# Optimization experiments

Measured on AMD Instinct MI355X. Metric: run time of the kernel, lower is better.

The kernel has to match this reference:

```python
import jax, jax.numpy as jnp
import numpy as np

L, S, R, NUM_RESNET = 6, 2, 3, 3
N = 2 ** L            # 64 blocks per axis
NX = N * S            # 128 grid points per axis
NCART_SIDE = 80
NCART = NCART_SIDE ** 2


def _perm_idx(L_, l):
    delta = 2 ** (L_ - l - 1)
    t = np.tile(np.arange(2) * delta, delta) + np.repeat(np.arange(delta), 2)
    t = np.tile(t, 2 ** l) + np.repeat(np.arange(2 ** l) * 2 ** (L_ - l), 2 ** (L_ - l))
    return jnp.asarray(t)


def _switch_idx(L_):
    h = L_ // 2
    t = np.tile(np.arange(2 ** h) * 2 ** h, 2 ** h) + np.repeat(np.arange(2 ** h), 2 ** h)
    return jnp.asarray(t)


def _bmm2(x, g_left, g_right):
    # x: (B,p,i,q,j). Right block-diag GEMM on (q,j), then left block-diag GEMM on (p,i).
    y = jnp.einsum('bpiqj,qjk->bpiqk', x, g_right)
    return jnp.einsum('bpiqk,pio->bpoqk', y, g_left)


def _complex_layer(xr, xi, p):
    # p: stacked (r1,i1,r2,i2,r3,i3,r4,i4); complex-style cross products of the original.
    r1, i1, r2, i2, r3, i3, r4, i4 = p
    yr = _bmm2(xr, r1, r1) + _bmm2(xr, i1, i1) + _bmm2(xi, r2, i2) + _bmm2(xi, i2, r2)
    yi = _bmm2(xi, r3, r3) + _bmm2(xi, i3, i3) + _bmm2(xr, r4, i4) + _bmm2(xr, i4, r4)
    return yr, yi


def _u_layer(xr, xi, p):
    ur1, ui1, ur2, ui2, ur3, ui3, ur4, ui4 = p
    return (_bmm2(xr, ur1, ur1) + _bmm2(xr, ui2, ui2)
            + _bmm2(xi, ur3, ui3) + _bmm2(xi, ui4, ur4))


def _permute(yr, yi, idx):
    yr = jnp.take(jnp.take(yr, idx, axis=1), idx, axis=3)
    yi = jnp.take(jnp.take(yi, idx, axis=1), idx, axis=3)
    return yr, yi


def _merge(y):  # (B,N,R,N,R) -> (B,N/2,2R,N/2,2R)
    return y.reshape(y.shape[0], N // 2, 2 * R, N // 2, 2 * R)


def _split(y):  # inverse of _merge
    return y.reshape(y.shape[0], N, R, N, R)


def reference(x, Vp, Hp, Mp, Gp, Up, cart_mat, r_index):
    B = x.shape[0]
    xr = x[..., 0].reshape(B, N, S, N, S)
    xi = x[..., 1].reshape(B, N, S, N, S)
    yr, yi = _complex_layer(xr, xi, Vp)                       # (B,N,R,N,R)
    for li, l in enumerate(range(L - 1, L // 2 - 1, -1)):     # H stages (permute then merge-GEMM)
        yr, yi = _permute(yr, yi, _perm_idx(L, l))
        yr, yi = _complex_layer(_merge(yr), _merge(yi), Hp[li])
        yr, yi = _split(yr), _split(yi)
    yr, yi = _permute(yr, yi, _switch_idx(L))                 # middle switch shuffle
    for k in range(NUM_RESNET):                               # residual M blocks
        zr, zi = _complex_layer(yr, yi, Mp[k])
        yr, yi = yr + zr, yi + zi
    for li, l in enumerate(range(L // 2 - 1, -1, -1)):        # G stages (merge-GEMM then permute)
        yr, yi = _complex_layer(_merge(yr), _merge(yi), Gp[li])
        yr, yi = _split(yr), _split(yi)
        yr, yi = _permute(yr, yi, _perm_idx(L, l))
    y = _u_layer(yr, yi, Up).reshape(B, NX * NX)              # real output, (B,NX,NX) flattened
    y = jnp.take(y, r_index, axis=1)                          # polar reindexing
    out = y @ cart_mat.T                                      # polar -> cartesian interpolation
    return out.reshape(B, NCART_SIDE, NCART_SIDE)


def setup_inputs() -> dict:
    key = jax.random.key(0)
    ks = jax.random.split(key, 9)
    B = 128
    x = jax.random.normal(ks[0], (B, NX, NX, 2), dtype=jnp.float32)
    Vp = jax.random.normal(ks[1], (8, N, S, R), dtype=jnp.float32) * 0.35
    Hp = jax.random.normal(ks[2], (L // 2, 8, N // 2, 2 * R, 2 * R), dtype=jnp.float32) * 0.2
    Mp = jax.random.normal(ks[3], (NUM_RESNET, 8, N, R, R), dtype=jnp.float32) * 0.25
    Gp = jax.random.normal(ks[4], (L // 2, 8, N // 2, 2 * R, 2 * R), dtype=jnp.float32) * 0.2
    Up = jax.random.normal(ks[5], (8, N, R, S), dtype=jnp.float32) * 0.35
    cart_mat = jax.random.normal(ks[6], (NCART, NX * NX), dtype=jnp.float32) * 0.01
    r_index = jax.random.permutation(ks[7], NX * NX).astype(jnp.int32)
    return {"x": x, "Vp": Vp, "Hp": Hp, "Mp": Mp, "Gp": Gp, "Up": Up,
            "cart_mat": cart_mat, "r_index": r_index}
```

## Files before the change

### kernel.cpp

```cpp
#include <hip/hip_runtime.h>


typedef __attribute__((ext_vector_type(8))) short sx8;
typedef __attribute__((ext_vector_type(4))) float fx4;
typedef __attribute__((ext_vector_type(8))) unsigned short usx8;
typedef __attribute__((ext_vector_type(4))) unsigned short usx4;

__device__ __forceinline__ unsigned short f2bf(float f) {
  unsigned u = __builtin_bit_cast(unsigned, f);
  u = (u + 0x7FFFu + ((u >> 16) & 1u)) >> 16;
  return (unsigned short)u;
}
__device__ __forceinline__ float bf2f(unsigned short h) {
  return __builtin_bit_cast(float, ((unsigned)h) << 16);
}

template<int ID>
__device__ __forceinline__ int rp_apply(int k) {
  if constexpr (ID == 0) { return k; }
  else if constexpr (ID == 3) { return (k & 7) * 8 + (k >> 3); }
  else {
    constexpr int l = (ID == 1) ? 4 : (ID == 2) ? 3 : (ID == 4) ? 2 : (ID == 5) ? 1 : 0;
    constexpr int d = 1 << (5 - l);
    constexpr int m2 = 2 * d;
    int g = k / m2, r = k % m2;
    return g * m2 + (r & 1) * d + (r >> 1);
  }
}

__global__ __launch_bounds__(256) void k_transpose(const float* __restrict__ x,
                                                   float* __restrict__ xtr,
                                                   float* __restrict__ xti) {
  __shared__ float ls[2][32][129];
  const int t = threadIdx.x;
  const int u = blockIdx.x;
  const int v0 = blockIdx.y * 32;
  for (int it = 0; it < 32; ++it) {
    int b = it * 4 + (t >> 6);
    int r = t & 63;
    int v = r >> 1, ch = r & 1;
    ls[ch][v][b] = x[(((size_t)b * 128 + u) * 128 + (v0 + v)) * 2 + ch];
  }
  __syncthreads();
  for (int it = 0; it < 32; ++it) {
    int idx = it * 256 + t;
    int ch = idx >> 12;
    int v = (idx >> 7) & 31;
    int b = idx & 127;
    float* dst = ch ? xti : xtr;
    dst[((size_t)(u * 128 + v0 + v)) * 128 + b] = ls[ch][v][b];
  }
}

__global__ __launch_bounds__(128) void k_vh(const float* __restrict__ xtr,
                                            const float* __restrict__ xti,
                                            float* __restrict__ yr,
                                            float* __restrict__ yi,
                                            const float* __restrict__ vp,
                                            const float* __restrict__ hp) {
  const int b = threadIdx.x;
  const int P = blockIdx.x, Q = blockIdx.y;
  float Vr[36], Vi[36];

#pragma unroll
  for (int pp = 0; pp < 2; ++pp)
#pragma unroll
    for (int qq = 0; qq < 2; ++qq) {
      const int p = 2 * P + pp, q = 2 * Q + qq;
      float Xr[4], Xi[4];
#pragma unroll
      for (int i = 0; i < 2; ++i)
#pragma unroll
        for (int j = 0; j < 2; ++j) {
          size_t off = ((size_t)((4 * P + 2 * pp + i) * 128 + (4 * Q + 2 * qq + j))) * 128 + b;
          Xr[i * 2 + j] = xtr[off];
          Xi[i * 2 + j] = xti[off];
        }
      float Ar[9], Ai[9];
#pragma unroll
      for (int k = 0; k < 9; ++k) { Ar[k] = 0.f; Ai[k] = 0.f; }
      auto termV = [&](float* Y, const float* X, int lm, int rm) {
        const float* Lw = vp + ((size_t)lm * 64 + p) * 6;
        const float* Rw = vp + ((size_t)rm * 64 + q) * 6;
#pragma unroll
        for (int i = 0; i < 2; ++i) {
          float t0 = X[i*2+0] * Rw[0] + X[i*2+1] * Rw[3];
          float t1 = X[i*2+0] * Rw[1] + X[i*2+1] * Rw[4];
          float t2 = X[i*2+0] * Rw[2] + X[i*2+1] * Rw[5];
#pragma unroll
          for (int o = 0; o < 3; ++o) {
            float lv = Lw[i * 3 + o];
            Y[o*3+0] += lv * t0; Y[o*3+1] += lv * t1; Y[o*3+2] += lv * t2;
          }
        }
      };
      termV(Ar, Xr, 0, 0); termV(Ar, Xr, 1, 1); termV(Ai, Xr, 6, 7); termV(Ai, Xr, 7, 6);
      termV(Ar, Xi, 2, 3); termV(Ar, Xi, 3, 2); termV(Ai, Xi, 4, 4); termV(Ai, Xi, 5, 5);
#pragma unroll
      for (int o = 0; o < 3; ++o)
#pragma unroll
        for (int k = 0; k < 3; ++k) {
          Vr[(3 * pp + o) * 6 + 3 * qq + k] = Ar[o * 3 + k];
          Vi[(3 * pp + o) * 6 + 3 * qq + k] = Ai[o * 3 + k];
        }
    }

  float Yr[36], Yi[36];
#pragma unroll
  for (int k = 0; k < 36; ++k) { Yr[k] = 0.f; Yi[k] = 0.f; }
  auto termH = [&](float* Y, const float* X, int lm, int rm) {
    const float* Lw = hp + ((size_t)lm * 32 + P) * 36;
    const float* Rw = hp + ((size_t)rm * 32 + Q) * 36;
#pragma unroll
    for (int i = 0; i < 6; ++i) {
      float tk[6];
#pragma unroll
      for (int k = 0; k < 6; ++k) tk[k] = 0.f;
#pragma unroll
      for (int j = 0; j < 6; ++j) {
        float xv = X[i * 6 + j];
#pragma unroll
        for (int k = 0; k < 6; ++k) tk[k] += xv * Rw[j * 6 + k];
      }
#pragma unroll
      for (int o = 0; o < 6; ++o) {
        float lv = Lw[i * 6 + o];
#pragma unroll
        for (int k = 0; k < 6; ++k) Y[o * 6 + k] += lv * tk[k];
      }
    }
  };
  termH(Yr, Vr, 0, 0); termH(Yr, Vr, 1, 1); termH(Yi, Vr, 6, 7); termH(Yi, Vr, 7, 6);
  termH(Yr, Vi, 2, 3); termH(Yr, Vi, 3, 2); termH(Yi, Vi, 4, 4); termH(Yi, Vi, 5, 5);

#pragma unroll
  for (int I = 0; I < 6; ++I)
#pragma unroll
    for (int J = 0; J < 6; ++J) {
      size_t off = ((size_t)((P * 6 + I) * 192 + (Q * 6 + J))) * 128 + b;
      yr[off] = Yr[I * 6 + J];
      yi[off] = Yi[I * 6 + J];
    }
}

template<int PERM>
__global__ __launch_bounds__(128) void k_hg(const float* __restrict__ xr,
                                            const float* __restrict__ xi,
                                            float* __restrict__ yr,
                                            float* __restrict__ yi,
                                            const float* __restrict__ wp) {
  const int b = threadIdx.x;
  const int P = blockIdx.x, Q = blockIdx.y;
  int rrow[6], rcol[6];
#pragma unroll
  for (int I = 0; I < 6; ++I) {
    rrow[I] = rp_apply<PERM>(2 * P + I / 3) * 3 + I % 3;
    rcol[I] = rp_apply<PERM>(2 * Q + I / 3) * 3 + I % 3;
  }
  float X[36], Yr[36], Yi[36];
#pragma unroll
  for (int k = 0; k < 36; ++k) { Yr[k] = 0.f; Yi[k] = 0.f; }

  auto loadX = [&](const float* src) {
#pragma unroll
    for (int I = 0; I < 6; ++I)
#pragma unroll
      for (int J = 0; J < 6; ++J)
        X[I * 6 + J] = src[((size_t)(rrow[I] * 192 + rcol[J])) * 128 + b];
  };
  auto term = [&](float* Y, int lm, int rm) {
    const float* Lw = wp + ((size_t)lm * 32 + P) * 36;
    const float* Rw = wp + ((size_t)rm * 32 + Q) * 36;
#pragma unroll
    for (int i = 0; i < 6; ++i) {
      float tk[6];
#pragma unroll
      for (int k = 0; k < 6; ++k) tk[k] = 0.f;
#pragma unroll
      for (int j = 0; j < 6; ++j) {
        float xv = X[i * 6 + j];
#pragma unroll
        for (int k = 0; k < 6; ++k) tk[k] += xv * Rw[j * 6 + k];
      }
#pragma unroll
      for (int o = 0; o < 6; ++o) {
        float lv = Lw[i * 6 + o];
#pragma unroll
        for (int k = 0; k < 6; ++k) Y[o * 6 + k] += lv * tk[k];
      }
    }
  };
  loadX(xr);
  term(Yr, 0, 0); term(Yr, 1, 1); term(Yi, 6, 7); term(Yi, 7, 6);
  loadX(xi);
  term(Yr, 2, 3); term(Yr, 3, 2); term(Yi, 4, 4); term(Yi, 5, 5);
#pragma unroll
  for (int I = 0; I < 6; ++I)
#pragma unroll
    for (int J = 0; J < 6; ++J) {
      size_t off = ((size_t)((P * 6 + I) * 192 + (Q * 6 + J))) * 128 + b;
      yr[off] = Yr[I * 6 + J];
      yi[off] = Yi[I * 6 + J];
    }
}

__global__ __launch_bounds__(128) void k_mg(const float* __restrict__ xr,
                                            const float* __restrict__ xi,
                                            float* __restrict__ yr,
                                            float* __restrict__ yi,
                                            const float* __restrict__ mp,
                                            const float* __restrict__ gp) {
  const int b = threadIdx.x;
  const int P = blockIdx.x, Q = blockIdx.y;
  float Vr[36], Vi[36];

#pragma unroll
  for (int aa = 0; aa < 2; ++aa)
#pragma unroll
    for (int bb = 0; bb < 2; ++bb) {
      const int p = 2 * P + aa, q = 2 * Q + bb;
      const int prow = rp_apply<3>(p) * 3, pcol = rp_apply<3>(q) * 3;
      float Xr[9], Xi[9];
#pragma unroll
      for (int i = 0; i < 3; ++i)
#pragma unroll
        for (int j = 0; j < 3; ++j) {
          size_t off = ((size_t)((prow + i) * 192 + (pcol + j))) * 128 + b;
          Xr[i * 3 + j] = xr[off];
          Xi[i * 3 + j] = xi[off];
        }
#pragma unroll
      for (int lk = 0; lk < 3; ++lk) {
        const float* wp = mp + (size_t)lk * (8 * 64 * 9);
        float Yr9[9], Yi9[9];
#pragma unroll
        for (int k = 0; k < 9; ++k) { Yr9[k] = Xr[k]; Yi9[k] = Xi[k]; }
        auto termM = [&](float* Y, const float* X, int lm, int rm) {
          const float* Lw = wp + ((size_t)lm * 64 + p) * 9;
          const float* Rw = wp + ((size_t)rm * 64 + q) * 9;
#pragma unroll
          for (int i = 0; i < 3; ++i) {
            float t0 = X[i*3+0] * Rw[0] + X[i*3+1] * Rw[3] + X[i*3+2] * Rw[6];
            float t1 = X[i*3+0] * Rw[1] + X[i*3+1] * Rw[4] + X[i*3+2] * Rw[7];
            float t2 = X[i*3+0] * Rw[2] + X[i*3+1] * Rw[5] + X[i*3+2] * Rw[8];
#pragma unroll
            for (int o = 0; o < 3; ++o) {
              float lv = Lw[i * 3 + o];
              Y[o*3+0] += lv * t0; Y[o*3+1] += lv * t1; Y[o*3+2] += lv * t2;
            }
          }
        };
        termM(Yr9, Xr, 0, 0); termM(Yr9, Xr, 1, 1); termM(Yi9, Xr, 6, 7); termM(Yi9, Xr, 7, 6);
        termM(Yr9, Xi, 2, 3); termM(Yr9, Xi, 3, 2); termM(Yi9, Xi, 4, 4); termM(Yi9, Xi, 5, 5);
#pragma unroll
        for (int k = 0; k < 9; ++k) { Xr[k] = Yr9[k]; Xi[k] = Yi9[k]; }
      }
#pragma unroll
      for (int i = 0; i < 3; ++i)
#pragma unroll
        for (int j = 0; j < 3; ++j) {
          Vr[(3 * aa + i) * 6 + 3 * bb + j] = Xr[i * 3 + j];
          Vi[(3 * aa + i) * 6 + 3 * bb + j] = Xi[i * 3 + j];
        }
    }

  float Yr[36], Yi[36];
#pragma unroll
  for (int k = 0; k < 36; ++k) { Yr[k] = 0.f; Yi[k] = 0.f; }
  auto termH = [&](float* Y, const float* X, int lm, int rm) {
    const float* Lw = gp + ((size_t)lm * 32 + P) * 36;
    const float* Rw = gp + ((size_t)rm * 32 + Q) * 36;
#pragma unroll
    for (int i = 0; i < 6; ++i) {
      float tk[6];
#pragma unroll
      for (int k = 0; k < 6; ++k) tk[k] = 0.f;
#pragma unroll
      for (int j = 0; j < 6; ++j) {
        float xv = X[i * 6 + j];
#pragma unroll
        for (int k = 0; k < 6; ++k) tk[k] += xv * Rw[j * 6 + k];
      }
#pragma unroll
      for (int o = 0; o < 6; ++o) {
        float lv = Lw[i * 6 + o];
#pragma unroll
        for (int k = 0; k < 6; ++k) Y[o * 6 + k] += lv * tk[k];
      }
    }
  };
  termH(Yr, Vr, 0, 0); termH(Yr, Vr, 1, 1); termH(Yi, Vr, 6, 7); termH(Yi, Vr, 7, 6);
  termH(Yr, Vi, 2, 3); termH(Yr, Vi, 3, 2); termH(Yi, Vi, 4, 4); termH(Yi, Vi, 5, 5);

#pragma unroll
  for (int I = 0; I < 6; ++I)
#pragma unroll
    for (int J = 0; J < 6; ++J) {
      size_t off = ((size_t)((P * 6 + I) * 192 + (Q * 6 + J))) * 128 + b;
      yr[off] = Yr[I * 6 + J];
      yi[off] = Yi[I * 6 + J];
    }
}

__global__ __launch_bounds__(128) void k_u(const float* __restrict__ xr,
                                           const float* __restrict__ xi,
                                           unsigned short* __restrict__ ut,
                                           const float* __restrict__ wp) {
  const int b = threadIdx.x;
  const int p = blockIdx.x, q = blockIdx.y;
  int rrow[3], rcol[3];
#pragma unroll
  for (int i = 0; i < 3; ++i) {
    rrow[i] = rp_apply<6>(p) * 3 + i;
    rcol[i] = rp_apply<6>(q) * 3 + i;
  }
  float X[9], Y[4] = {0.f, 0.f, 0.f, 0.f};
  auto loadX = [&](const float* src) {
#pragma unroll
    for (int i = 0; i < 3; ++i)
#pragma unroll
      for (int j = 0; j < 3; ++j)
        X[i * 3 + j] = src[((size_t)(rrow[i] * 192 + rcol[j])) * 128 + b];
  };
  auto term = [&](int lm, int rm) {
    const float* Lw = wp + ((size_t)lm * 64 + p) * 6;
    const float* Rw = wp + ((size_t)rm * 64 + q) * 6;
#pragma unroll
    for (int i = 0; i < 3; ++i) {
      float t0 = X[i*3+0] * Rw[0] + X[i*3+1] * Rw[2] + X[i*3+2] * Rw[4];
      float t1 = X[i*3+0] * Rw[1] + X[i*3+1] * Rw[3] + X[i*3+2] * Rw[5];
      Y[0] += Lw[i*2+0] * t0; Y[1] += Lw[i*2+0] * t1;
      Y[2] += Lw[i*2+1] * t0; Y[3] += Lw[i*2+1] * t1;
    }
  };
  loadX(xr); term(0, 0); term(3, 3);
  loadX(xi); term(4, 5); term(7, 6);
#pragma unroll
  for (int o = 0; o < 2; ++o)
#pragma unroll
    for (int k = 0; k < 2; ++k)
      ut[((size_t)((p * 2 + o) * 128 + (q * 2 + k))) * 128 + b] = f2bf(Y[o * 2 + k]);
}

__global__ __launch_bounds__(256) void k_gather(const unsigned short* __restrict__ ut,
                                                const int* __restrict__ r_index,
                                                unsigned short* __restrict__ yg) {
  __shared__ unsigned short ls[64][130];
  __shared__ int ridx[64];
  const int t = threadIdx.x;
  const int m0 = blockIdx.x * 64;
  if (t < 64) ridx[t] = r_index[m0 + t];
  __syncthreads();
  for (int it = 0; it < 32; ++it) {
    int idx = it * 256 + t;
    int ml = idx >> 7, b = idx & 127;
    ls[ml][b] = ut[(size_t)ridx[ml] * 128 + b];
  }
  __syncthreads();
  int b = t >> 1, half = t & 1;
#pragma unroll
  for (int c = 0; c < 4; ++c) {
    usx8 v;
#pragma unroll
    for (int e = 0; e < 8; ++e) v[e] = ls[half * 32 + c * 8 + e][b];
    *(usx8*)(yg + (size_t)b * 16384 + m0 + half * 32 + c * 8) = v;
  }
}

#define GEMM_KC 16
#define GEMM_NKS 32

__global__ __launch_bounds__(256) void k_gemm(const unsigned short* __restrict__ yg,
                                              const float* __restrict__ cart,
                                              unsigned short* __restrict__ partial) {
  __shared__ unsigned short As[2][128][40];
  __shared__ unsigned short Bs[2][128][40];
  const int t = threadIdx.x;
  const int lane = t & 63, w = t >> 6;
  const int wm = w >> 1, wn = w & 1;
  const int c0 = blockIdx.x * 128;
  const int k0 = blockIdx.y * 1024;
  const int kc = blockIdx.y;

  fx4 acc[4][4];
#pragma unroll
  for (int i = 0; i < 4; ++i)
#pragma unroll
    for (int j = 0; j < 4; ++j) acc[i][j] = (fx4)0.f;

  auto ldA = [&](int rep, int kpos) -> usx8 {
    int c = t + rep * 256;
    return *(const usx8*)(yg + (size_t)(c >> 2) * 16384 + kpos + (c & 3) * 8);
  };
  auto stA = [&](int buf, int rep, usx8 v) {
    int c = t + rep * 256;
    *(usx8*)(&As[buf][c >> 2][(c & 3) * 8]) = v;
  };
  auto ldB = [&](int rep, int kpos) -> fx4 {
    int c = t + rep * 256;
    return *(const fx4*)(cart + (size_t)(c0 + (c >> 3)) * 16384 + kpos + (c & 7) * 4);
  };
  auto stB = [&](int buf, int rep, fx4 f) {
    int c = t + rep * 256;
    usx4 v;
    v[0] = f2bf(f[0]); v[1] = f2bf(f[1]); v[2] = f2bf(f[2]); v[3] = f2bf(f[3]);
    *(usx4*)(&Bs[buf][c >> 3][(c & 7) * 4]) = v;
  };

  {
    usx8 a0 = ldA(0, k0), a1 = ldA(1, k0);
    fx4 b0 = ldB(0, k0), b1 = ldB(1, k0), b2 = ldB(2, k0), b3 = ldB(3, k0);
    stA(0, 0, a0); stA(0, 1, a1);
    stB(0, 0, b0); stB(0, 1, b1); stB(0, 2, b2); stB(0, 3, b3);
  }
  __syncthreads();

  for (int s = 0; s < GEMM_NKS; ++s) {
    const int cur = s & 1;
    usx8 av0, av1; fx4 bv0, bv1, bv2, bv3;
    const bool pf = (s + 1 < GEMM_NKS);
    if (pf) {
      int kpos = k0 + (s + 1) * 32;
      av0 = ldA(0, kpos); av1 = ldA(1, kpos);
      bv0 = ldB(0, kpos); bv1 = ldB(1, kpos); bv2 = ldB(2, kpos); bv3 = ldB(3, kpos);
    }
    sx8 af[4], bfr[4];
#pragma unroll
    for (int mi = 0; mi < 4; ++mi) {
      int row = wm * 64 + mi * 16 + (lane & 15);
      af[mi] = *(const sx8*)(&As[cur][row][(lane >> 4) * 8]);
    }
#pragma unroll
    for (int ni = 0; ni < 4; ++ni) {
      int row = wn * 64 + ni * 16 + (lane & 15);
      bfr[ni] = *(const sx8*)(&Bs[cur][row][(lane >> 4) * 8]);
    }
#pragma unroll
    for (int mi = 0; mi < 4; ++mi)
#pragma unroll
      for (int ni = 0; ni < 4; ++ni)
        acc[mi][ni] = __builtin_amdgcn_mfma_f32_16x16x32_bf16(af[mi], bfr[ni], acc[mi][ni], 0, 0, 0);
    if (pf) {
      stA(cur ^ 1, 0, av0); stA(cur ^ 1, 1, av1);
      stB(cur ^ 1, 0, bv0); stB(cur ^ 1, 1, bv1); stB(cur ^ 1, 2, bv2); stB(cur ^ 1, 3, bv3);
    }
    __syncthreads();
  }

#pragma unroll
  for (int mi = 0; mi < 4; ++mi) {
    int brow = wm * 64 + mi * 16 + (lane >> 4) * 4;
#pragma unroll
    for (int ni = 0; ni < 4; ++ni) {
      int cc = c0 + wn * 64 + ni * 16 + (lane & 15);
#pragma unroll
      for (int r = 0; r < 4; ++r)
        partial[((size_t)kc * 128 + brow + r) * 6400 + cc] = f2bf(acc[mi][ni][r]);
    }
  }
}

__global__ __launch_bounds__(256) void k_reduce(const unsigned short* __restrict__ partial,
                                                float* __restrict__ out) {
  int i = blockIdx.x * 256 + threadIdx.x;
  fx4 s = (fx4)0.f;
#pragma unroll
  for (int kc = 0; kc < GEMM_KC; ++kc) {
    usx4 v = *(const usx4*)(partial + (size_t)kc * 819200 + (size_t)i * 4);
    s[0] += bf2f(v[0]); s[1] += bf2f(v[1]); s[2] += bf2f(v[2]); s[3] += bf2f(v[3]);
  }
  *(fx4*)(out + (size_t)i * 4) = s;
}

extern "C" void kernel_launch(void* const* d_in, const int* in_sizes, int n_in,
                              void* d_out, int out_size, void* d_ws, size_t ws_size,
                              hipStream_t stream) {
  const float* x    = (const float*)d_in[0];
  const float* Vp   = (const float*)d_in[1];
  const float* Hp   = (const float*)d_in[2];
  const float* Mp   = (const float*)d_in[3];
  const float* Gp   = (const float*)d_in[4];
  const float* Up   = (const float*)d_in[5];
  const float* cart = (const float*)d_in[6];
  const int*   ridx = (const int*)d_in[7];
  float* out = (float*)d_out;
  float* ws  = (float*)d_ws;

  const size_t PSZ = 4718592;
  float* P0r = ws;
  float* P0i = ws + PSZ;
  float* P1r = ws + 2 * PSZ;
  float* P1i = ws + 3 * PSZ;
  float* xtr = ws + 4 * PSZ;
  float* xti = xtr + 2097152;
  unsigned short* ut = (unsigned short*)(ws + 4 * PSZ);
  unsigned short* yg = (unsigned short*)(ws + 4 * PSZ + 1048576);
  unsigned short* partial = (unsigned short*)ws;

  const size_t HSZ = 8 * 32 * 36;

  k_transpose<<<dim3(128, 4), 256, 0, stream>>>(x, xtr, xti);
  k_vh<<<dim3(32, 32), 128, 0, stream>>>(xtr, xti, P0r, P0i, Vp, Hp + 0 * HSZ);
  k_hg<1><<<dim3(32, 32), 128, 0, stream>>>(P0r, P0i, P1r, P1i, Hp + 1 * HSZ);
  k_hg<2><<<dim3(32, 32), 128, 0, stream>>>(P1r, P1i, P0r, P0i, Hp + 2 * HSZ);
  k_mg<<<dim3(32, 32), 128, 0, stream>>>(P0r, P0i, P1r, P1i, Mp, Gp + 0 * HSZ);
  k_hg<4><<<dim3(32, 32), 128, 0, stream>>>(P1r, P1i, P0r, P0i, Gp + 1 * HSZ);
  k_hg<5><<<dim3(32, 32), 128, 0, stream>>>(P0r, P0i, P1r, P1i, Gp + 2 * HSZ);
  k_u<<<dim3(64, 64), 128, 0, stream>>>(P1r, P1i, ut, Up);
  k_gather<<<dim3(256), 256, 0, stream>>>(ut, ridx, yg);
  k_gemm<<<dim3(50, GEMM_KC), 256, 0, stream>>>(yg, cart, partial);
  k_reduce<<<dim3(800), 256, 0, stream>>>(partial, out);
  (void)in_sizes; (void)n_in; (void)out_size; (void)ws_size;
}
```

Measured before the change: 360.4 us.

## Retile final GEMM with narrower N tiles, deeper K steps, fewer fp32 split-K partials

The polar-to-cartesian GEMM is re-tiled from 128x128 output tiles with 16-way split-K to 128x64 tiles with 4-way split-K and a K step of 64 per stage. Each wave now owns a 32-row strip, and partials are stored as fp32 instead of bf16, which shrinks the reduce to four reads per element. The aim is to cut partial-sum traffic and make better use of the cart matrix loads. The trade-off is a grid of 400 blocks instead of 800, and each A tile is reused across only 64 columns, so yg is re-read more often.

```diff
diff --git a/kernel.cpp b/kernel.cpp
--- a/kernel.cpp
+++ b/kernel.cpp
@@ -367,108 +367,114 @@
   }
 }
 
-#define GEMM_KC 16
-#define GEMM_NKS 32
-
-__global__ __launch_bounds__(256) void k_gemm(const unsigned short* __restrict__ yg,
-                                              const float* __restrict__ cart,
-                                              unsigned short* __restrict__ partial) {
-  __shared__ unsigned short As[2][128][40];
-  __shared__ unsigned short Bs[2][128][40];
+#define G2_KC 4
+#define G2_STEPS 64
+#define G2_PITCH 72
+
+__global__ __launch_bounds__(256) void k_gemm2(const unsigned short* __restrict__ yg,
+                                               const float* __restrict__ cart,
+                                               float* __restrict__ partial) {
+  __shared__ unsigned short As[2][128][G2_PITCH];
+  __shared__ unsigned short Bs[2][64][G2_PITCH];
   const int t = threadIdx.x;
   const int lane = t & 63, w = t >> 6;
-  const int wm = w >> 1, wn = w & 1;
-  const int c0 = blockIdx.x * 128;
-  const int k0 = blockIdx.y * 1024;
-  const int kc = blockIdx.y;
-
-  fx4 acc[4][4];
-#pragma unroll
-  for (int i = 0; i < 4; ++i)
+  const int kc = blockIdx.x;
+  const int c0 = blockIdx.y * 64;
+  const int k0 = kc * 4096;
+
+  fx4 acc[2][4];
+#pragma unroll
+  for (int i = 0; i < 2; ++i)
 #pragma unroll
     for (int j = 0; j < 4; ++j) acc[i][j] = (fx4)0.f;
 
   auto ldA = [&](int rep, int kpos) -> usx8 {
     int c = t + rep * 256;
-    return *(const usx8*)(yg + (size_t)(c >> 2) * 16384 + kpos + (c & 3) * 8);
+    return *(const usx8*)(yg + (size_t)(c >> 3) * 16384 + kpos + (c & 7) * 8);
   };
   auto stA = [&](int buf, int rep, usx8 v) {
     int c = t + rep * 256;
-    *(usx8*)(&As[buf][c >> 2][(c & 3) * 8]) = v;
-  };
-  auto ldB = [&](int rep, int kpos) -> fx4 {
+    *(usx8*)(&As[buf][c >> 3][(c & 7) * 8]) = v;
+  };
+  auto ldB = [&](int rep, int kpos, fx4* f0, fx4* f1) {
     int c = t + rep * 256;
-    return *(const fx4*)(cart + (size_t)(c0 + (c >> 3)) * 16384 + kpos + (c & 7) * 4);
-  };
-  auto stB = [&](int buf, int rep, fx4 f) {
+    const float* p = cart + (size_t)(c0 + (c >> 3)) * 16384 + kpos + (c & 7) * 8;
+    *f0 = *(const fx4*)p;
+    *f1 = *(const fx4*)(p + 4);
+  };
+  auto stB = [&](int buf, int rep, fx4 f0, fx4 f1) {
     int c = t + rep * 256;
-    usx4 v;
-    v[0] = f2bf(f[0]); v[1] = f2bf(f[1]); v[2] = f2bf(f[2]); v[3] = f2bf(f[3]);
-    *(usx4*)(&Bs[buf][c >> 3][(c & 7) * 4]) = v;
+    usx8 v;
+    v[0]=f2bf(f0[0]); v[1]=f2bf(f0[1]); v[2]=f2bf(f0[2]); v[3]=f2bf(f0[3]);
+    v[4]=f2bf(f1[0]); v[5]=f2bf(f1[1]); v[6]=f2bf(f1[2]); v[7]=f2bf(f1[3]);
+    *(usx8*)(&Bs[buf][c >> 3][(c & 7) * 8]) = v;
   };
 
   {
-    usx8 a0 = ldA(0, k0), a1 = ldA(1, k0);
-    fx4 b0 = ldB(0, k0), b1 = ldB(1, k0), b2 = ldB(2, k0), b3 = ldB(3, k0);
-    stA(0, 0, a0); stA(0, 1, a1);
-    stB(0, 0, b0); stB(0, 1, b1); stB(0, 2, b2); stB(0, 3, b3);
+    usx8 a0 = ldA(0, k0), a1 = ldA(1, k0), a2 = ldA(2, k0), a3 = ldA(3, k0);
+    fx4 b00, b01, b10, b11;
+    ldB(0, k0, &b00, &b01); ldB(1, k0, &b10, &b11);
+    stA(0, 0, a0); stA(0, 1, a1); stA(0, 2, a2); stA(0, 3, a3);
+    stB(0, 0, b00, b01); stB(0, 1, b10, b11);
   }
   __syncthreads();
 
-  for (int s = 0; s < GEMM_NKS; ++s) {
+  for (int s = 0; s < G2_STEPS; ++s) {
     const int cur = s & 1;
-    usx8 av0, av1; fx4 bv0, bv1, bv2, bv3;
-    const bool pf = (s + 1 < GEMM_NKS);
+    usx8 av[4]; fx4 b00, b01, b10, b11;
+    const bool pf = (s + 1 < G2_STEPS);
     if (pf) {
-      int kpos = k0 + (s + 1) * 32;
-      av0 = ldA(0, kpos); av1 = ldA(1, kpos);
-      bv0 = ldB(0, kpos); bv1 = ldB(1, kpos); bv2 = ldB(2, kpos); bv3 = ldB(3, kpos);
-    }
-    sx8 af[4], bfr[4];
-#pragma unroll
-    for (int mi = 0; mi < 4; ++mi) {
-      int row = wm * 64 + mi * 16 + (lane & 15);
-      af[mi] = *(const sx8*)(&As[cur][row][(lane >> 4) * 8]);
-    }
+      int kpos = k0 + (s + 1) * 64;
+      av[0] = ldA(0, kpos); av[1] = ldA(1, kpos);
+      av[2] = ldA(2, kpos); av[3] = ldA(3, kpos);
+      ldB(0, kpos, &b00, &b01); ldB(1, kpos, &b10, &b11);
+    }
+    sx8 af[2][2], bf[4][2];
+#pragma unroll
+    for (int mi = 0; mi < 2; ++mi)
+#pragma unroll
+      for (int kk = 0; kk < 2; ++kk)
+        af[mi][kk] = *(const sx8*)(&As[cur][w * 32 + mi * 16 + (lane & 15)][kk * 32 + (lane >> 4) * 8]);
+#pragma unroll
+    for (int ni = 0; ni < 4; ++ni)
+#pragma unroll
+      for (int kk = 0; kk < 2; ++kk)
+        bf[ni][kk] = *(const sx8*)(&Bs[cur][ni * 16 + (lane & 15)][kk * 32 + (lane >> 4) * 8]);
+#pragma unroll
+    for (int kk = 0; kk < 2; ++kk)
+#pragma unroll
+      for (int mi = 0; mi < 2; ++mi)
+#pragma unroll
+        for (int ni = 0; ni < 4; ++ni)
+          acc[mi][ni] = __builtin_amdgcn_mfma_f32_16x16x32_bf16(af[mi][kk], bf[ni][kk], acc[mi][ni], 0, 0, 0);
+    if (pf) {
+      stA(cur ^ 1, 0, av[0]); stA(cur ^ 1, 1, av[1]);
+      stA(cur ^ 1, 2, av[2]); stA(cur ^ 1, 3, av[3]);
+      stB(cur ^ 1, 0, b00, b01); stB(cur ^ 1, 1, b10, b11);
+    }
+    __syncthreads();
+  }
+
+#pragma unroll
+  for (int mi = 0; mi < 2; ++mi) {
+    int brow = w * 32 + mi * 16 + (lane >> 4) * 4;
 #pragma unroll
     for (int ni = 0; ni < 4; ++ni) {
-      int row = wn * 64 + ni * 16 + (lane & 15);
-      bfr[ni] = *(const sx8*)(&Bs[cur][row][(lane >> 4) * 8]);
-    }
-#pragma unroll
-    for (int mi = 0; mi < 4; ++mi)
-#pragma unroll
-      for (int ni = 0; ni < 4; ++ni)
-        acc[mi][ni] = __builtin_amdgcn_mfma_f32_16x16x32_bf16(af[mi], bfr[ni], acc[mi][ni], 0, 0, 0);
-    if (pf) {
-      stA(cur ^ 1, 0, av0); stA(cur ^ 1, 1, av1);
-      stB(cur ^ 1, 0, bv0); stB(cur ^ 1, 1, bv1); stB(cur ^ 1, 2, bv2); stB(cur ^ 1, 3, bv3);
-    }
-    __syncthreads();
-  }
-
-#pragma unroll
-  for (int mi = 0; mi < 4; ++mi) {
-    int brow = wm * 64 + mi * 16 + (lane >> 4) * 4;
-#pragma unroll
-    for (int ni = 0; ni < 4; ++ni) {
-      int cc = c0 + wn * 64 + ni * 16 + (lane & 15);
+      int cc = c0 + ni * 16 + (lane & 15);
 #pragma unroll
       for (int r = 0; r < 4; ++r)
-        partial[((size_t)kc * 128 + brow + r) * 6400 + cc] = f2bf(acc[mi][ni][r]);
-    }
-  }
-}
-
-__global__ __launch_bounds__(256) void k_reduce(const unsigned short* __restrict__ partial,
-                                                float* __restrict__ out) {
+        partial[((size_t)kc * 128 + brow + r) * 6400 + cc] = acc[mi][ni][r];
+    }
+  }
+}
+
+__global__ __launch_bounds__(256) void k_reduce2(const float* __restrict__ partial,
+                                                 float* __restrict__ out) {
   int i = blockIdx.x * 256 + threadIdx.x;
   fx4 s = (fx4)0.f;
 #pragma unroll
-  for (int kc = 0; kc < GEMM_KC; ++kc) {
-    usx4 v = *(const usx4*)(partial + (size_t)kc * 819200 + (size_t)i * 4);
-    s[0] += bf2f(v[0]); s[1] += bf2f(v[1]); s[2] += bf2f(v[2]); s[3] += bf2f(v[3]);
-  }
+  for (int kc = 0; kc < G2_KC; ++kc)
+    s += *(const fx4*)(partial + (size_t)kc * 819200 + (size_t)i * 4);
   *(fx4*)(out + (size_t)i * 4) = s;
 }
 
@@ -495,7 +501,7 @@
   float* xti = xtr + 2097152;
   unsigned short* ut = (unsigned short*)(ws + 4 * PSZ);
   unsigned short* yg = (unsigned short*)(ws + 4 * PSZ + 1048576);
-  unsigned short* partial = (unsigned short*)ws;
+  float* partial = ws;
 
   const size_t HSZ = 8 * 32 * 36;
 
@@ -508,7 +514,7 @@
   k_hg<5><<<dim3(32, 32), 128, 0, stream>>>(P0r, P0i, P1r, P1i, Gp + 2 * HSZ);
   k_u<<<dim3(64, 64), 128, 0, stream>>>(P1r, P1i, ut, Up);
   k_gather<<<dim3(256), 256, 0, stream>>>(ut, ridx, yg);
-  k_gemm<<<dim3(50, GEMM_KC), 256, 0, stream>>>(yg, cart, partial);
-  k_reduce<<<dim3(800), 256, 0, stream>>>(partial, out);
+  k_gemm2<<<dim3(G2_KC, 100), 256, 0, stream>>>(yg, cart, partial);
+  k_reduce2<<<dim3(800), 256, 0, stream>>>(partial, out);
   (void)in_sizes; (void)n_in; (void)out_size; (void)ws_size;
 }
```

Result: faster. 342.4 us (-5.0%).
